# Performance work log

Measured on AMD Instinct MI355X. Metric: run time of the kernel, lower is better.

The kernel has to match this reference:

```python
import jax, jax.numpy as jnp
import numpy as np

B, C = 8, 2048          # batch, out_dim (projection channels)
HG = WG = 32            # global crop feature map
HL = WL = 12            # local crop feature map
STUDENT_TEMP = 0.1
TEMP_SCHEDULE = np.concatenate([np.linspace(0.04, 0.07, 30), np.ones(100 - 30) * 0.07])

# Fixed relative boxes (x1, x2, y1, y2) per (iq, v) crop pair, shared across the
# batch so grid shapes are static. Source computes grid_H from teacher_feat.shape[0]
# (= C, a quirk of the original code) and grid_W from shape[1] (= spatial H); boxes
# are chosen so resulting grids are ~[22-25, 22-24].
PAIRS = [
    (0, 1, (-0.80, 0.70, -0.500, -0.475), (-0.90, 0.60, -0.60, 0.60)),
    (0, 2, (-0.75, 0.75,  0.100,  0.125), (-0.80, 0.80, -0.80, 0.80)),
    (0, 3, (-0.60, 0.90, -0.200, -0.178), (-0.70, 0.90, -0.90, 0.70)),
    (1, 0, (-0.70, 0.80,  0.300,  0.322), (-0.85, 0.65, -0.50, 0.90)),
    (1, 2, (-0.90, 0.50, -0.100, -0.076), (-0.60, 0.95, -0.95, 0.60)),
    (1, 3, (-0.50, 0.95,  0.200,  0.224), (-0.90, 0.90, -0.40, 0.95)),
]


def _grid_dims(box, Hc, Wc):
    x1, x2, y1, y2 = box
    return int(abs(y1 - y2) / 2 * Hc), int(abs(x1 - x2) / 2 * Wc)  # (grid_H, grid_W)


def _make_grid(box, gH, gW):
    # Faithful to source: meshgrid([linspace(y1,y2,gH), linspace(x1,x2,gW)]),
    # stacked so channel 0 holds the y-linspace (which grid_sample reads as x).
    x1, x2, y1, y2 = box
    yy, xx = jnp.meshgrid(jnp.linspace(y1, y2, gH), jnp.linspace(x1, x2, gW), indexing='ij')
    return jnp.stack([yy, xx], axis=-1)  # [gH, gW, 2]


def _grid_sample_border(img, grid):
    # torch.nn.functional.grid_sample, bilinear, padding_mode='border',
    # align_corners=False. img: [B, C, H, W], grid: [gH, gW, 2] (same grid per batch).
    H, W = img.shape[-2], img.shape[-1]
    gx, gy = grid[..., 0], grid[..., 1]
    ix = jnp.clip((gx + 1.0) * (W * 0.5) - 0.5, 0.0, W - 1.0)  # border: clip coords
    iy = jnp.clip((gy + 1.0) * (H * 0.5) - 0.5, 0.0, H - 1.0)
    x0f, y0f = jnp.floor(ix), jnp.floor(iy)
    wx = (ix - x0f)[None, None]  # [1,1,gH,gW]
    wy = (iy - y0f)[None, None]
    x0 = x0f.astype(jnp.int32)
    y0 = y0f.astype(jnp.int32)
    x1 = jnp.minimum(x0 + 1, W - 1)
    y1 = jnp.minimum(y0 + 1, H - 1)
    v00 = img[:, :, y0, x0]
    v01 = img[:, :, y0, x1]
    v10 = img[:, :, y1, x0]
    v11 = img[:, :, y1, x1]
    return (1.0 - wy) * ((1.0 - wx) * v00 + wx * v01) + wy * ((1.0 - wx) * v10 + wx * v11)


def setup_inputs() -> dict:
    key = jax.random.key(0)
    ks = jax.random.split(key, 7)
    return {
        'student_g0': jax.random.normal(ks[0], (B, C, HG, WG), jnp.float32),
        'student_g1': jax.random.normal(ks[1], (B, C, HG, WG), jnp.float32),
        'student_l0': jax.random.normal(ks[2], (B, C, HL, WL), jnp.float32),
        'student_l1': jax.random.normal(ks[3], (B, C, HL, WL), jnp.float32),
        'teacher_g0': jax.random.normal(ks[4], (B, C, HG, WG), jnp.float32),
        'teacher_g1': jax.random.normal(ks[5], (B, C, HG, WG), jnp.float32),
        'center': jax.random.normal(ks[6], (1, C), jnp.float32) * 0.1,
        'epoch': 5,
    }


def reference(student_g0, student_g1, student_l0, student_l1,
              teacher_g0, teacher_g1, center, epoch):
    temp = float(TEMP_SCHEDULE[epoch])
    students = [s / STUDENT_TEMP for s in (student_g0, student_g1, student_l0, student_l1)]
    cen = center[:, :, None, None]  # [1,C,1,1]
    cteach = [jax.nn.softmax((t - cen) / temp, axis=1) for t in (teacher_g0, teacher_g1)]

    losses = []
    for iq, v, tbox, sbox in PAIRS:
        tfeat = cteach[iq]   # [B,C,H,W]
        sfeat = students[v]  # [B,C,h,w]
        # Faithful: source passes (shape[0]=C, shape[1]=spatial H) as (H, W).
        gH, gW = _grid_dims(tbox, C, tfeat.shape[2])
        t_common = jax.lax.stop_gradient(_grid_sample_border(tfeat, _make_grid(tbox, gH, gW)))
        s_common = _grid_sample_border(sfeat, _make_grid(sbox, gH, gW))
        # cross-entropy over channels -> [B, gH, gW]
        loss = (-t_common * jax.nn.log_softmax(s_common, axis=1)).sum(axis=1)
        losses.append(loss.reshape(-1))
    return jnp.concatenate(losses).mean()
```

## Files before the change

kernel.cpp:

```cpp
#include <hip/hip_runtime.h>
#include <hip/hip_fp16.h>

#define NPOS 26688

struct PairInfo {
  int iq, v, Hs, gH, gW, base, per;
  unsigned magicPer, magicW;
  int tOfs, tN, tCb;
  int sN, sCb;
  float tx1, tx2, ty1, ty2;
  float sx1, sx2, sy1, sy2;
};

__constant__ PairInfo g_pairs[6] = {
  {0,1,32,25,24,    0,600, 7158279u,178956971u,    0,2, 7, 22,5, -0.80f,0.70f,-0.500f,-0.475f,  -0.90f,0.60f,-0.60f,0.60f},
  {0,2,12,25,24, 4800,600, 7158279u,178956971u,  512,2,17, 12,0, -0.75f,0.75f, 0.100f, 0.125f,  -0.80f,0.80f,-0.80f,0.80f},
  {0,3,12,22,24, 9600,528, 8134408u,178956971u, 1024,2,12, 12,0, -0.60f,0.90f,-0.200f,-0.178f,  -0.70f,0.90f,-0.90f,0.70f},
  {1,0,32,22,24,13824,528, 8134408u,178956971u, 1536,2,20, 24,7, -0.70f,0.80f, 0.300f, 0.322f,  -0.85f,0.65f,-0.50f,0.90f},
  {1,2,12,24,22,18048,528, 8134408u,195225787u, 2048,3,13, 12,0, -0.90f,0.50f,-0.100f,-0.076f,  -0.60f,0.95f,-0.95f,0.60f},
  {1,3,12,24,23,22272,552, 7780739u,186737709u, 2816,3,18, 12,0, -0.50f,0.95f, 0.200f, 0.224f,  -0.90f,0.90f,-0.40f,0.95f},
};

__constant__ int g_ux[2][32] = {
  {-1,-1,-1,-1,-1,-1,-1, 0, 1,-1,-1,-1, 2, 3,-1,-1,-1, 4, 5,-1,-1,-1,-1,-1,-1,-1,-1,-1,-1,-1,-1,-1},
  {-1,-1,-1,-1,-1,-1,-1,-1,-1,-1,-1,-1,-1, 0, 1, 2,-1,-1, 3, 4, 5, 6,-1,-1,-1,-1,-1,-1,-1,-1,-1,-1},
};
__constant__ int g_tentX[2][8] = {
  { 7, 8,12,13,17,18,-100,-100},
  {13,14,15,18,19,20,  20,  21},
};
__constant__ int g_tentO[2][8] = {
  {   0,   0,1024,1024, 512, 512,   0,   0},
  {2048,2048,2048,2816,2816,2816,1536,1536},
};
__constant__ int g_tentN[2][8] = {
  {2,2,2,2,2,2,2,2},
  {3,3,3,3,3,3,2,2},
};
__constant__ int g_tentC[2][8] = {
  {0,1,0,1,0,1,0,0},
  {0,1,2,0,1,2,0,1},
};
__constant__ int g_cumTex[6] = {0, 512, 1024, 1536, 2048, 2816};
__constant__ int g_tN[6]    = {2, 2, 2, 2, 3, 3};
__constant__ int g_tCb[6]   = {7, 17, 12, 20, 13, 18};

__device__ inline float get_invtemp(const int* __restrict__ ep) {
  int e = ep[0];
  e = e < 0 ? 0 : (e > 99 ? 99 : e);
  float temp = (e < 30) ? (0.04f + (float)e * (0.03f / 29.0f)) : 0.07f;
  return 1.0f / temp;
}

__device__ inline float sel4(const float4& v, int q) {
  return q == 0 ? v.x : q == 1 ? v.y : q == 2 ? v.z : v.w;
}

typedef _Float16 hv2 __attribute__((ext_vector_type(2)));
__device__ inline float fdot2f(__half2 a, __half2 b, float c) {
#if defined(__has_builtin)
#if __has_builtin(__builtin_amdgcn_fdot2)
  return __builtin_amdgcn_fdot2(*reinterpret_cast<hv2*>(&a),
                                *reinterpret_cast<hv2*>(&b), c, false);
#else
  float2 af = __half22float2(a), bf = __half22float2(b);
  return fmaf(af.x, bf.x, fmaf(af.y, bf.y, c));
#endif
#else
  float2 af = __half22float2(a), bf = __half22float2(b);
  return fmaf(af.x, bf.x, fmaf(af.y, bf.y, c));
#endif
}

__global__ __launch_bounds__(256) void dino_phase1(
    const float* __restrict__ tg0, const float* __restrict__ tg1,
    const float* __restrict__ cen, const int* __restrict__ ep,
    float* __restrict__ part_m, float* __restrict__ part_s,
    __half* __restrict__ Tc,
    const float* __restrict__ sl0, const float* __restrict__ sl1,
    __half* __restrict__ Sl0, __half* __restrict__ Sl1,
    const float* __restrict__ sg0, const float* __restrict__ sg1,
    __half* __restrict__ Sg0, __half* __restrict__ Sg1) {
  __shared__ float smem[7424];
  int bid = blockIdx.x;
  int t = threadIdx.x;

  if (bid < 1024) {
    int cg = bid & 63;
    int b = (bid >> 6) & 7;
    int view = bid >> 9;
    const float* __restrict__ src = view ? tg1 : tg0;
    float invtemp = get_invtemp(ep);
    float* cenl = smem + 7392;
    if (t < 32) cenl[t] = cen[cg * 32 + t];
    __syncthreads();

    int y = t >> 3, x0 = (t & 7) * 4;
    int y33 = y * 33;
    int s0 = g_ux[view][x0], s1 = g_ux[view][x0 + 1];
    int s2 = g_ux[view][x0 + 2], s3 = g_ux[view][x0 + 3];
    const float* base = src + ((size_t)(b * 2048 + cg * 32)) * 1024 + t * 4;

    float4 m4 = make_float4(-1e30f, -1e30f, -1e30f, -1e30f);
    float4 s4 = make_float4(0.f, 0.f, 0.f, 0.f);
#pragma unroll 4
    for (int c = 0; c < 32; ++c) {
      float4 v = *reinterpret_cast<const float4*>(base + (size_t)c * 1024);
      float cv = cenl[c];
      float4 lg;
      lg.x = (v.x - cv) * invtemp; lg.y = (v.y - cv) * invtemp;
      lg.z = (v.z - cv) * invtemp; lg.w = (v.w - cv) * invtemp;
      if (s0 >= 0) smem[s0 * 1056 + y33 + c] = lg.x;
      if (s1 >= 0) smem[s1 * 1056 + y33 + c] = lg.y;
      if (s2 >= 0) smem[s2 * 1056 + y33 + c] = lg.z;
      if (s3 >= 0) smem[s3 * 1056 + y33 + c] = lg.w;
      float mn;
      mn = fmaxf(m4.x, lg.x); s4.x = s4.x * __expf(m4.x - mn) + __expf(lg.x - mn); m4.x = mn;
      mn = fmaxf(m4.y, lg.y); s4.y = s4.y * __expf(m4.y - mn) + __expf(lg.y - mn); m4.y = mn;
      mn = fmaxf(m4.z, lg.z); s4.z = s4.z * __expf(m4.z - mn) + __expf(lg.z - mn); m4.z = mn;
      mn = fmaxf(m4.w, lg.w); s4.w = s4.w * __expf(m4.w - mn) + __expf(lg.w - mn); m4.w = mn;
    }
    size_t prow = ((size_t)((view * 8 + b) * 64 + cg)) * 1024 + t * 4;
    *reinterpret_cast<float4*>(part_m + prow) = m4;
    *reinterpret_cast<float4*>(part_s + prow) = s4;

#pragma unroll
    for (int e = 0; e < 8; ++e) {
      int ex = g_tentX[view][e];
      int d = ex - x0;
      if (d >= 0 && d < 4) {
        int slot = g_ux[view][ex];
        float mm = sel4(m4, d);
        int tex = g_tentO[view][e] + (b * 32 + y) * g_tentN[view][e] + g_tentC[view][e];
        tex = min(max(tex, 0), 3583);
        __half hv[32];
#pragma unroll
        for (int c = 0; c < 32; ++c)
          hv[c] = __float2half(smem[slot * 1056 + y33 + c] - mm);
        uint4* dst = reinterpret_cast<uint4*>(Tc + (size_t)tex * 2048 + cg * 32);
        const uint4* sv = reinterpret_cast<const uint4*>(hv);
        dst[0] = sv[0]; dst[1] = sv[1]; dst[2] = sv[2]; dst[3] = sv[3];
      }
    }
    return;
  }

  if (bid < 3072) {
    float* tile = smem;
    int lb = bid - 1024;
    int ct = lb & 127;
    int g = lb >> 7;
    int b = g & 7;
    int vv = g >> 3;
    const float* __restrict__ src = vv ? sl1 : sl0;
    __half* __restrict__ dst = vv ? Sl1 : Sl0;
    const float* sp = src + ((size_t)(b * 2048 + ct * 16)) * 144;
#pragma unroll
    for (int k = 0; k < 9; ++k) {
      int idx = t + 256 * k;
      int c = idx / 144;
      int yx = idx - c * 144;
      tile[c * 145 + yx] = sp[idx] * 10.f;
    }
    __syncthreads();
    __half* dp = dst + ((size_t)(b * 144)) * 2048 + ct * 16;
#pragma unroll
    for (int k = 0; k < 2; ++k) {
      int u = t + 256 * k;
      if (u < 288) {
        int yx = u >> 1, q8 = (u & 1) * 8;
        __half hv[8];
#pragma unroll
        for (int j = 0; j < 8; ++j) hv[j] = __float2half(tile[(q8 + j) * 145 + yx]);
        *reinterpret_cast<float4*>(dp + (size_t)yx * 2048 + q8) =
            *reinterpret_cast<float4*>(hv);
      }
    }
    return;
  }

  float* tile = smem;
  int lb = bid - 3072;
  int ct = lb & 31;
  int t2 = lb >> 5;
  int yi = t2 % 26;
  int g = t2 / 26;
  int y = yi + 1;
  int b = g & 7;
  int which = g >> 3;
  const float* __restrict__ src = which ? sg1 : sg0;
  __half* __restrict__ dst = which ? Sg1 : Sg0;
  int cb = which ? 5 : 7;
  int n = which ? 22 : 24;

  int xg = t & 7, ch = t >> 3;
  const float* sp = src + (((size_t)(b * 2048 + ct * 64 + ch)) * 32 + y) * 32 + xg * 4;
  float4 v0 = *reinterpret_cast<const float4*>(sp);
  float4 v1 = *reinterpret_cast<const float4*>(sp + 32768);
  tile[ch * 33 + xg * 4 + 0] = v0.x * 10.f;
  tile[ch * 33 + xg * 4 + 1] = v0.y * 10.f;
  tile[ch * 33 + xg * 4 + 2] = v0.z * 10.f;
  tile[ch * 33 + xg * 4 + 3] = v0.w * 10.f;
  tile[(ch + 32) * 33 + xg * 4 + 0] = v1.x * 10.f;
  tile[(ch + 32) * 33 + xg * 4 + 1] = v1.y * 10.f;
  tile[(ch + 32) * 33 + xg * 4 + 2] = v1.z * 10.f;
  tile[(ch + 32) * 33 + xg * 4 + 3] = v1.w * 10.f;
  __syncthreads();
  int xx = t >> 3, ccq = (t & 7) * 8;
  if (xx >= cb && xx < cb + n) {
    __half hv[8];
#pragma unroll
    for (int j = 0; j < 8; ++j) hv[j] = __float2half(tile[(ccq + j) * 33 + xx]);
    __half* dp = dst + ((size_t)((b * 32 + y) * n + (xx - cb))) * 2048 + ct * 64 + ccq;
    *reinterpret_cast<float4*>(dp) = *reinterpret_cast<float4*>(hv);
  }
}

union H8 { uint4 u; __half2 h[4]; };

__global__ __launch_bounds__(256) void dino_probs(
    const __half* __restrict__ Tc, __half* __restrict__ Tp,
    const float* __restrict__ part_m, const float* __restrict__ part_s) {
  __shared__ float pr[66];
  int bid = blockIdx.x;
  int t = threadIdx.x;
  int p = 0;
#pragma unroll
  for (int q = 1; q < 6; ++q) p += (bid >= g_cumTex[q]) ? 1 : 0;
  int r = bid - g_cumTex[p];
  int n = g_tN[p];
  int by = (n == 2) ? (r >> 1) : (r / 3);
  by = min(max(by, 0), 255);
  int ci = min(max(r - by * n, 0), n - 1);
  int x = g_tCb[p] + ci;
  int view = (p >= 3) ? 1 : 0;
  int b = by >> 5, y = by & 31;
  int vb = view * 8 + b;

  if (t < 64) {
    float mg = part_m[((size_t)(vb * 64 + t)) * 1024 + y * 32 + x];
    float sg = part_s[((size_t)(vb * 64 + t)) * 1024 + y * 32 + x];
    pr[t] = mg;
    float M = mg;
#pragma unroll
    for (int off = 32; off; off >>= 1) M = fmaxf(M, __shfl_xor(M, off));
    float sv = sg * __expf(mg - M);
#pragma unroll
    for (int off = 32; off; off >>= 1) sv += __shfl_xor(sv, off);
    if (t == 0) { pr[64] = M; pr[65] = 1.f / sv; }
  }
  __syncthreads();
  float off = pr[t >> 2] - pr[64];
  float invS = pr[65];

  int tex = min(g_cumTex[p] + by * n + ci, 3583);
  size_t base = (size_t)tex * 2048 + t * 8;
  H8 hh;
  hh.u = *reinterpret_cast<const uint4*>(Tc + base);
#pragma unroll
  for (int pc = 0; pc < 4; ++pc) {
    float2 f = __half22float2(hh.h[pc]);
    f.x = __expf(f.x + off) * invS;
    f.y = __expf(f.y + off) * invS;
    hh.h[pc] = __floats2half2_rn(f.x, f.y);
  }
  *reinterpret_cast<uint4*>(Tp + base) = hh.u;
}

__global__ __launch_bounds__(256) void dino_main(
    const __half* __restrict__ Tp,
    const __half* __restrict__ S0, const __half* __restrict__ S1,
    const __half* __restrict__ S2, const __half* __restrict__ S3,
    float* __restrict__ losses) {
  int wid = threadIdx.x >> 6, lane = threadIdx.x & 63;
  int pair = blockIdx.x / 1200;
  int slot = blockIdx.x - pair * 1200;
  PairInfo pi = g_pairs[pair];
  int posInPair = slot * 4 + wid;
  if (posInPair >= pi.per * 8) return;

  unsigned up = (unsigned)posInPair;
  int b = (int)__umulhi(up, pi.magicPer);
  b = min(max(b, 0), 7);
  int r = posInPair - b * pi.per;
  r = min(max(r, 0), pi.per - 1);
  int i = (int)__umulhi((unsigned)r, pi.magicW);
  i = min(max(i, 0), pi.gH - 1);
  int j = r - i * pi.gW;
  j = min(max(j, 0), pi.gW - 1);

  float tyy = pi.ty1 + (float)i * (pi.ty2 - pi.ty1) / (float)(pi.gH - 1);
  float txx = pi.tx1 + (float)j * (pi.tx2 - pi.tx1) / (float)(pi.gW - 1);
  float tix = fminf(fmaxf((tyy + 1.0f) * 16.0f - 0.5f, 0.0f), 31.0f);
  float tiy = fminf(fmaxf((txx + 1.0f) * 16.0f - 0.5f, 0.0f), 31.0f);
  int tx0 = (int)tix, ty0 = (int)tiy;
  float wxt = tix - (float)tx0, wyt = tiy - (float)ty0;
  int tx1i = min(tx0 + 1, 31), ty1i = min(ty0 + 1, 31);

  int hs = pi.Hs;
  float hh = 0.5f * (float)hs, hm = (float)(hs - 1);
  float syy = pi.sy1 + (float)i * (pi.sy2 - pi.sy1) / (float)(pi.gH - 1);
  float sxx = pi.sx1 + (float)j * (pi.sx2 - pi.sx1) / (float)(pi.gW - 1);
  float six = fminf(fmaxf((syy + 1.0f) * hh - 0.5f, 0.0f), hm);
  float siy = fminf(fmaxf((sxx + 1.0f) * hh - 0.5f, 0.0f), hm);
  int sx0 = (int)six, sy0 = (int)siy;
  float wxs = six - (float)sx0, wys = siy - (float)sy0;
  int sx1i = min(sx0 + 1, hs - 1), sy1i = min(sy0 + 1, hs - 1);

  const __half* __restrict__ S =
      (pi.v == 0) ? S0 : (pi.v == 1) ? S1 : (pi.v == 2) ? S2 : S3;

  int tc0 = min(max(tx0 - pi.tCb, 0), pi.tN - 1);
  int tc1 = min(max(tx1i - pi.tCb, 0), pi.tN - 1);
  int trow = pi.tOfs + (b * 32 + ty0) * pi.tN;
  int trow1 = pi.tOfs + (b * 32 + ty1i) * pi.tN;
  int toff00 = min(trow + tc0, 3583) * 2048;
  int toff01 = min(trow + tc1, 3583) * 2048;
  int toff10 = min(trow1 + tc0, 3583) * 2048;
  int toff11 = min(trow1 + tc1, 3583) * 2048;
  int sc0 = min(max(sx0 - pi.sCb, 0), pi.sN - 1);
  int sc1 = min(max(sx1i - pi.sCb, 0), pi.sN - 1);
  int soff00 = ((b * hs + sy0) * pi.sN + sc0) * 2048;
  int soff01 = ((b * hs + sy0) * pi.sN + sc1) * 2048;
  int soff10 = ((b * hs + sy1i) * pi.sN + sc0) * 2048;
  int soff11 = ((b * hs + sy1i) * pi.sN + sc1) * 2048;

  __half2 wt00 = __float2half2_rn((1.f - wyt) * (1.f - wxt));
  __half2 wt01 = __float2half2_rn((1.f - wyt) * wxt);
  __half2 wt10 = __float2half2_rn(wyt * (1.f - wxt));
  __half2 wt11 = __float2half2_rn(wyt * wxt);
  __half2 ws00 = __float2half2_rn((1.f - wys) * (1.f - wxs));
  __half2 ws01 = __float2half2_rn((1.f - wys) * wxs);
  __half2 ws10 = __float2half2_rn(wys * (1.f - wxs));
  __half2 ws11 = __float2half2_rn(wys * wxs);

  float sum = 0.f, dot = 0.f;
#pragma unroll
  for (int k = 0; k < 4; ++k) {
    int c0 = (k << 9) + (lane << 3);
    H8 t00, t01, t10, t11, a00, a01, a10, a11;
    t00.u = *reinterpret_cast<const uint4*>(Tp + toff00 + c0);
    t01.u = *reinterpret_cast<const uint4*>(Tp + toff01 + c0);
    t10.u = *reinterpret_cast<const uint4*>(Tp + toff10 + c0);
    t11.u = *reinterpret_cast<const uint4*>(Tp + toff11 + c0);
    a00.u = *reinterpret_cast<const uint4*>(S + soff00 + c0);
    a01.u = *reinterpret_cast<const uint4*>(S + soff01 + c0);
    a10.u = *reinterpret_cast<const uint4*>(S + soff10 + c0);
    a11.u = *reinterpret_cast<const uint4*>(S + soff11 + c0);
#pragma unroll
    for (int p = 0; p < 4; ++p) {
      __half2 tc2 = __hmul2(wt00, t00.h[p]);
      tc2 = __hfma2(wt01, t01.h[p], tc2);
      tc2 = __hfma2(wt10, t10.h[p], tc2);
      tc2 = __hfma2(wt11, t11.h[p], tc2);
      __half2 sc2 = __hmul2(ws00, a00.h[p]);
      sc2 = __hfma2(ws01, a01.h[p], sc2);
      sc2 = __hfma2(ws10, a10.h[p], sc2);
      sc2 = __hfma2(ws11, a11.h[p], sc2);
      dot = fdot2f(tc2, sc2, dot);
      float2 scf = __half22float2(sc2);
      sum += __expf(scf.x);
      sum += __expf(scf.y);
    }
  }
#pragma unroll
  for (int off = 32; off; off >>= 1) {
    sum += __shfl_down(sum, off);
    dot += __shfl_down(dot, off);
  }
  if (lane == 0) losses[pi.base + posInPair] = logf(sum) - dot;
}

__global__ __launch_bounds__(1024) void dino_reduce(const float* __restrict__ losses,
                                                    float* __restrict__ out) {
  __shared__ double sd[1024];
  int t = threadIdx.x;
  double a = 0.0;
  for (int i4 = t; i4 < 6672; i4 += 1024) {
    float4 v = *reinterpret_cast<const float4*>(losses + i4 * 4);
    a += (double)v.x + (double)v.y + (double)v.z + (double)v.w;
  }
  sd[t] = a;
  __syncthreads();
  for (int off = 512; off; off >>= 1) {
    if (t < off) sd[t] += sd[t + off];
    __syncthreads();
  }
  if (t == 0) out[0] = (float)(sd[0] / (double)NPOS);
}

extern "C" void kernel_launch(void* const* d_in, const int* in_sizes, int n_in,
                              void* d_out, int out_size, void* d_ws, size_t ws_size,
                              hipStream_t stream) {
  const float* sg0 = (const float*)d_in[0];
  const float* sg1 = (const float*)d_in[1];
  const float* sl0 = (const float*)d_in[2];
  const float* sl1 = (const float*)d_in[3];
  const float* tg0 = (const float*)d_in[4];
  const float* tg1 = (const float*)d_in[5];
  const float* cen = (const float*)d_in[6];
  const int* epoch = (const int*)d_in[7];
  float* out = (float*)d_out;
  char* w = (char*)d_ws;

  const size_t OFF_LOSS= 131072;
  const size_t OFF_PM  = 262144;
  const size_t OFF_PS  = 4456448;
  const size_t OFF_TC  = 8650752;
  const size_t OFF_TP  = 23330816;
  const size_t OFF_SG0 = 38010880;
  const size_t OFF_SG1 = 63176704;
  const size_t OFF_SL0 = 86245376;
  const size_t OFF_SL1 = 90963968;

  float* losses = (float*)(w + OFF_LOSS);
  float* part_m = (float*)(w + OFF_PM);
  float* part_s = (float*)(w + OFF_PS);
  __half* Tc  = (__half*)(w + OFF_TC);
  __half* Tp  = (__half*)(w + OFF_TP);
  __half* Sg0 = (__half*)(w + OFF_SG0);
  __half* Sg1 = (__half*)(w + OFF_SG1);
  __half* Sl0 = (__half*)(w + OFF_SL0);
  __half* Sl1 = (__half*)(w + OFF_SL1);

  dino_phase1<<<16384, 256, 0, stream>>>(tg0, tg1, cen, epoch, part_m, part_s, Tc,
                                         sl0, sl1, Sl0, Sl1, sg0, sg1, Sg0, Sg1);
  dino_probs<<<3584, 256, 0, stream>>>(Tc, Tp, part_m, part_s);
  dino_main<<<7200, 256, 0, stream>>>(Tp, Sg0, Sg1, Sl0, Sl1, losses);
  dino_reduce<<<1, 1024, 0, stream>>>(losses, out);
}
```

Measured before the change: 122.6 us.

## Compute teacher softmax only at sampled columns instead of full per-pixel partial stats

Phase 1 no longer computes online max/sum partials over every teacher pixel. It only gathers the raw fp32 teacher values at the few x-columns the grid samples. The probs kernel now does the full channel softmax (with centering and temperature) per sampled position, in one block-wide reduction. The global-student transpose is also restructured to process 16 channels by the full 32x32 map per block, so far fewer phase-1 blocks are launched. This removes the exp-heavy work and the part_m/part_s traffic for unused pixels, at the cost of a larger fp32 intermediate buffer.

After: 142.2 us. +16.0%, slower.

```diff
diff --git a/kernel.cpp b/kernel.cpp
--- a/kernel.cpp
+++ b/kernel.cpp
@@ -25,35 +25,17 @@
   {-1,-1,-1,-1,-1,-1,-1, 0, 1,-1,-1,-1, 2, 3,-1,-1,-1, 4, 5,-1,-1,-1,-1,-1,-1,-1,-1,-1,-1,-1,-1,-1},
   {-1,-1,-1,-1,-1,-1,-1,-1,-1,-1,-1,-1,-1, 0, 1, 2,-1,-1, 3, 4, 5, 6,-1,-1,-1,-1,-1,-1,-1,-1,-1,-1},
 };
-__constant__ int g_tentX[2][8] = {
-  { 7, 8,12,13,17,18,-100,-100},
-  {13,14,15,18,19,20,  20,  21},
-};
-__constant__ int g_tentO[2][8] = {
-  {   0,   0,1024,1024, 512, 512,   0,   0},
-  {2048,2048,2048,2816,2816,2816,1536,1536},
-};
-__constant__ int g_tentN[2][8] = {
-  {2,2,2,2,2,2,2,2},
-  {3,3,3,3,3,3,2,2},
-};
-__constant__ int g_tentC[2][8] = {
-  {0,1,0,1,0,1,0,0},
-  {0,1,2,0,1,2,0,1},
-};
-__constant__ int g_cumTex[6] = {0, 512, 1024, 1536, 2048, 2816};
-__constant__ int g_tN[6]    = {2, 2, 2, 2, 3, 3};
-__constant__ int g_tCb[6]   = {7, 17, 12, 20, 13, 18};
+__constant__ int g_weSlot[2][8] = {{0,1,2,3,4,5,0,0},{0,1,2,3,4,5,5,6}};
+__constant__ int g_weBase[2][8] = {{0,1,1024,1025,512,513,0,0},
+                                   {2048,2049,2050,2816,2817,2818,1536,1537}};
+__constant__ int g_weStr[2][8]  = {{2,2,2,2,2,2,2,2},{3,3,3,3,3,3,2,2}};
+__constant__ int g_weN[2] = {6, 8};
 
 __device__ inline float get_invtemp(const int* __restrict__ ep) {
   int e = ep[0];
   e = e < 0 ? 0 : (e > 99 ? 99 : e);
   float temp = (e < 30) ? (0.04f + (float)e * (0.03f / 29.0f)) : 0.07f;
   return 1.0f / temp;
-}
-
-__device__ inline float sel4(const float4& v, int q) {
-  return q == 0 ? v.x : q == 1 ? v.y : q == 2 ? v.z : v.w;
 }
 
 typedef _Float16 hv2 __attribute__((ext_vector_type(2)));
@@ -74,198 +56,184 @@
 
 __global__ __launch_bounds__(256) void dino_phase1(
     const float* __restrict__ tg0, const float* __restrict__ tg1,
-    const float* __restrict__ cen, const int* __restrict__ ep,
-    float* __restrict__ part_m, float* __restrict__ part_s,
-    __half* __restrict__ Tc,
+    float* __restrict__ Tcf,
+    const float* __restrict__ sg0, const float* __restrict__ sg1,
+    __half* __restrict__ Sg0, __half* __restrict__ Sg1,
     const float* __restrict__ sl0, const float* __restrict__ sl1,
-    __half* __restrict__ Sl0, __half* __restrict__ Sl1,
-    const float* __restrict__ sg0, const float* __restrict__ sg1,
-    __half* __restrict__ Sg0, __half* __restrict__ Sg1) {
-  __shared__ float smem[7424];
+    __half* __restrict__ Sl0, __half* __restrict__ Sl1) {
+  __shared__ float smem[5700];
   int bid = blockIdx.x;
   int t = threadIdx.x;
 
-  if (bid < 1024) {
-    int cg = bid & 63;
-    int b = (bid >> 6) & 7;
-    int view = bid >> 9;
+  if (bid < 2048) {
+    int cg = bid & 127;
+    int b = (bid >> 7) & 7;
+    int view = bid >> 10;
     const float* __restrict__ src = view ? tg1 : tg0;
-    float invtemp = get_invtemp(ep);
-    float* cenl = smem + 7392;
-    if (t < 32) cenl[t] = cen[cg * 32 + t];
+    const float* base = src + ((size_t)(b * 2048 + cg * 16)) * 1024;
+#pragma unroll
+    for (int k = 0; k < 16; ++k) {
+      int idx = k * 256 + t;
+      int c = idx >> 8, p4 = idx & 255;
+      int y = p4 >> 3, x0 = (p4 & 7) * 4;
+      float4 v = *reinterpret_cast<const float4*>(base + (size_t)c * 1024 + p4 * 4);
+      int s0 = g_ux[view][x0],     s1 = g_ux[view][x0 + 1];
+      int s2 = g_ux[view][x0 + 2], s3 = g_ux[view][x0 + 3];
+      if (s0 >= 0) smem[s0 * 544 + y * 17 + c] = v.x;
+      if (s1 >= 0) smem[s1 * 544 + y * 17 + c] = v.y;
+      if (s2 >= 0) smem[s2 * 544 + y * 17 + c] = v.z;
+      if (s3 >= 0) smem[s3 * 544 + y * 17 + c] = v.w;
+    }
     __syncthreads();
-
-    int y = t >> 3, x0 = (t & 7) * 4;
-    int y33 = y * 33;
-    int s0 = g_ux[view][x0], s1 = g_ux[view][x0 + 1];
-    int s2 = g_ux[view][x0 + 2], s3 = g_ux[view][x0 + 3];
-    const float* base = src + ((size_t)(b * 2048 + cg * 32)) * 1024 + t * 4;
-
-    float4 m4 = make_float4(-1e30f, -1e30f, -1e30f, -1e30f);
-    float4 s4 = make_float4(0.f, 0.f, 0.f, 0.f);
-#pragma unroll 4
-    for (int c = 0; c < 32; ++c) {
-      float4 v = *reinterpret_cast<const float4*>(base + (size_t)c * 1024);
-      float cv = cenl[c];
-      float4 lg;
-      lg.x = (v.x - cv) * invtemp; lg.y = (v.y - cv) * invtemp;
-      lg.z = (v.z - cv) * invtemp; lg.w = (v.w - cv) * invtemp;
-      if (s0 >= 0) smem[s0 * 1056 + y33 + c] = lg.x;
-      if (s1 >= 0) smem[s1 * 1056 + y33 + c] = lg.y;
-      if (s2 >= 0) smem[s2 * 1056 + y33 + c] = lg.z;
-      if (s3 >= 0) smem[s3 * 1056 + y33 + c] = lg.w;
-      float mn;
-      mn = fmaxf(m4.x, lg.x); s4.x = s4.x * __expf(m4.x - mn) + __expf(lg.x - mn); m4.x = mn;
-      mn = fmaxf(m4.y, lg.y); s4.y = s4.y * __expf(m4.y - mn) + __expf(lg.y - mn); m4.y = mn;
-      mn = fmaxf(m4.z, lg.z); s4.z = s4.z * __expf(m4.z - mn) + __expf(lg.z - mn); m4.z = mn;
-      mn = fmaxf(m4.w, lg.w); s4.w = s4.w * __expf(m4.w - mn) + __expf(lg.w - mn); m4.w = mn;
-    }
-    size_t prow = ((size_t)((view * 8 + b) * 64 + cg)) * 1024 + t * 4;
-    *reinterpret_cast<float4*>(part_m + prow) = m4;
-    *reinterpret_cast<float4*>(part_s + prow) = s4;
-
-#pragma unroll
-    for (int e = 0; e < 8; ++e) {
-      int ex = g_tentX[view][e];
-      int d = ex - x0;
-      if (d >= 0 && d < 4) {
-        int slot = g_ux[view][ex];
-        float mm = sel4(m4, d);
-        int tex = g_tentO[view][e] + (b * 32 + y) * g_tentN[view][e] + g_tentC[view][e];
-        tex = min(max(tex, 0), 3583);
-        __half hv[32];
-#pragma unroll
-        for (int c = 0; c < 32; ++c)
-          hv[c] = __float2half(smem[slot * 1056 + y33 + c] - mm);
-        uint4* dst = reinterpret_cast<uint4*>(Tc + (size_t)tex * 2048 + cg * 32);
-        const uint4* sv = reinterpret_cast<const uint4*>(hv);
-        dst[0] = sv[0]; dst[1] = sv[1]; dst[2] = sv[2]; dst[3] = sv[3];
+    int nw = g_weN[view];
+    if (t < nw * 32) {
+      int e = t >> 5, y = t & 31;
+      int slot = g_weSlot[view][e];
+      int tex = g_weBase[view][e] + (b * 32 + y) * g_weStr[view][e];
+      tex = min(max(tex, 0), 3583);
+      float arr[16];
+#pragma unroll
+      for (int c = 0; c < 16; ++c) arr[c] = smem[slot * 544 + y * 17 + c];
+      float* dp = Tcf + (size_t)tex * 2048 + cg * 16;
+#pragma unroll
+      for (int q = 0; q < 4; ++q)
+        *reinterpret_cast<float4*>(dp + q * 4) =
+            make_float4(arr[4 * q], arr[4 * q + 1], arr[4 * q + 2], arr[4 * q + 3]);
+    }
+    return;
+  }
+
+  if (bid < 4096) {
+    int lb = bid - 2048;
+    int cg = lb & 127;
+    int b = (lb >> 7) & 7;
+    int which = lb >> 10;
+    const float* __restrict__ src = which ? sg1 : sg0;
+    __half* __restrict__ dst = which ? Sg1 : Sg0;
+    int cb = which ? 5 : 7;
+    int n = which ? 22 : 24;
+    unsigned magicN = which ? 195225787u : 178956971u;
+    const float* base = src + ((size_t)(b * 2048 + cg * 16)) * 1024;
+    __half* hlds = reinterpret_cast<__half*>(smem);
+#pragma unroll
+    for (int k = 0; k < 16; ++k) {
+      int idx = k * 256 + t;
+      int c = idx >> 8, p4 = idx & 255;
+      int y = p4 >> 3, x0 = (p4 & 7) * 4;
+      float4 v = *reinterpret_cast<const float4*>(base + (size_t)c * 1024 + p4 * 4);
+      if (y >= 1 && y <= 26) {
+        int rb = (y - 1) * n - cb;
+#pragma unroll
+        for (int q = 0; q < 4; ++q) {
+          int x = x0 + q;
+          if (x >= cb && x < cb + n) {
+            float val = (q == 0) ? v.x : (q == 1) ? v.y : (q == 2) ? v.z : v.w;
+            hlds[(rb + x) * 18 + c] = __float2half(val * 10.f);
+          }
+        }
       }
     }
+    __syncthreads();
+    int total = 26 * n;
+    const unsigned* hw = reinterpret_cast<const unsigned*>(smem);
+#pragma unroll
+    for (int k2 = 0; k2 < 3; ++k2) {
+      int u = t + 256 * k2;
+      if (u < total) {
+        int yy = (int)__umulhi((unsigned)u, magicN);
+        int cx = u - yy * n;
+        int y = yy + 1;
+        unsigned r[8];
+#pragma unroll
+        for (int q = 0; q < 8; ++q) r[q] = hw[u * 9 + q];
+        unsigned* dp = reinterpret_cast<unsigned*>(
+            dst + ((size_t)((b * 32 + y) * n + cx)) * 2048 + cg * 16);
+        *reinterpret_cast<uint4*>(dp) = make_uint4(r[0], r[1], r[2], r[3]);
+        *reinterpret_cast<uint4*>(dp + 4) = make_uint4(r[4], r[5], r[6], r[7]);
+      }
+    }
     return;
   }
 
-  if (bid < 3072) {
-    float* tile = smem;
-    int lb = bid - 1024;
-    int ct = lb & 127;
-    int g = lb >> 7;
-    int b = g & 7;
-    int vv = g >> 3;
-    const float* __restrict__ src = vv ? sl1 : sl0;
-    __half* __restrict__ dst = vv ? Sl1 : Sl0;
-    const float* sp = src + ((size_t)(b * 2048 + ct * 16)) * 144;
-#pragma unroll
-    for (int k = 0; k < 9; ++k) {
-      int idx = t + 256 * k;
-      int c = idx / 144;
-      int yx = idx - c * 144;
-      tile[c * 145 + yx] = sp[idx] * 10.f;
-    }
-    __syncthreads();
-    __half* dp = dst + ((size_t)(b * 144)) * 2048 + ct * 16;
-#pragma unroll
-    for (int k = 0; k < 2; ++k) {
-      int u = t + 256 * k;
-      if (u < 288) {
-        int yx = u >> 1, q8 = (u & 1) * 8;
-        __half hv[8];
-#pragma unroll
-        for (int j = 0; j < 8; ++j) hv[j] = __float2half(tile[(q8 + j) * 145 + yx]);
-        *reinterpret_cast<float4*>(dp + (size_t)yx * 2048 + q8) =
-            *reinterpret_cast<float4*>(hv);
-      }
-    }
-    return;
-  }
-
   float* tile = smem;
-  int lb = bid - 3072;
-  int ct = lb & 31;
-  int t2 = lb >> 5;
-  int yi = t2 % 26;
-  int g = t2 / 26;
-  int y = yi + 1;
+  int lb = bid - 4096;
+  int ct = lb & 127;
+  int g = lb >> 7;
   int b = g & 7;
-  int which = g >> 3;
-  const float* __restrict__ src = which ? sg1 : sg0;
-  __half* __restrict__ dst = which ? Sg1 : Sg0;
-  int cb = which ? 5 : 7;
-  int n = which ? 22 : 24;
-
-  int xg = t & 7, ch = t >> 3;
-  const float* sp = src + (((size_t)(b * 2048 + ct * 64 + ch)) * 32 + y) * 32 + xg * 4;
-  float4 v0 = *reinterpret_cast<const float4*>(sp);
-  float4 v1 = *reinterpret_cast<const float4*>(sp + 32768);
-  tile[ch * 33 + xg * 4 + 0] = v0.x * 10.f;
-  tile[ch * 33 + xg * 4 + 1] = v0.y * 10.f;
-  tile[ch * 33 + xg * 4 + 2] = v0.z * 10.f;
-  tile[ch * 33 + xg * 4 + 3] = v0.w * 10.f;
-  tile[(ch + 32) * 33 + xg * 4 + 0] = v1.x * 10.f;
-  tile[(ch + 32) * 33 + xg * 4 + 1] = v1.y * 10.f;
-  tile[(ch + 32) * 33 + xg * 4 + 2] = v1.z * 10.f;
-  tile[(ch + 32) * 33 + xg * 4 + 3] = v1.w * 10.f;
+  int vv = g >> 3;
+  const float* __restrict__ src = vv ? sl1 : sl0;
+  __half* __restrict__ dst = vv ? Sl1 : Sl0;
+  const float* sp = src + ((size_t)(b * 2048 + ct * 16)) * 144;
+#pragma unroll
+  for (int k = 0; k < 9; ++k) {
+    int idx = t + 256 * k;
+    int c = idx / 144;
+    int yx = idx - c * 144;
+    tile[c * 145 + yx] = sp[idx] * 10.f;
+  }
   __syncthreads();
-  int xx = t >> 3, ccq = (t & 7) * 8;
-  if (xx >= cb && xx < cb + n) {
-    __half hv[8];
-#pragma unroll
-    for (int j = 0; j < 8; ++j) hv[j] = __float2half(tile[(ccq + j) * 33 + xx]);
-    __half* dp = dst + ((size_t)((b * 32 + y) * n + (xx - cb))) * 2048 + ct * 64 + ccq;
-    *reinterpret_cast<float4*>(dp) = *reinterpret_cast<float4*>(hv);
-  }
+  __half* dp = dst + ((size_t)(b * 144)) * 2048 + ct * 16;
+#pragma unroll
+  for (int k = 0; k < 2; ++k) {
+    int u = t + 256 * k;
+    if (u < 288) {
+      int yx = u >> 1, q8 = (u & 1) * 8;
+      __half hv[8];
+#pragma unroll
+      for (int j = 0; j < 8; ++j) hv[j] = __float2half(tile[(q8 + j) * 145 + yx]);
+      *reinterpret_cast<float4*>(dp + (size_t)yx * 2048 + q8) =
+          *reinterpret_cast<float4*>(hv);
+    }
+  }
+}
+
+__global__ __launch_bounds__(256) void dino_probs(
+    const float* __restrict__ Tcf, __half* __restrict__ Tp,
+    const float* __restrict__ cen, const int* __restrict__ ep) {
+  __shared__ float rm[4], rs[4];
+  int tex = blockIdx.x;
+  int t = threadIdx.x;
+  int lane = t & 63, w = t >> 6;
+  float invtemp = get_invtemp(ep);
+
+  const float* cp = Tcf + (size_t)tex * 2048 + t * 8;
+  float4 v0 = *reinterpret_cast<const float4*>(cp);
+  float4 v1 = *reinterpret_cast<const float4*>(cp + 4);
+  float4 c0 = *reinterpret_cast<const float4*>(cen + t * 8);
+  float4 c1 = *reinterpret_cast<const float4*>(cen + t * 8 + 4);
+  float lg[8];
+  lg[0] = (v0.x - c0.x) * invtemp; lg[1] = (v0.y - c0.y) * invtemp;
+  lg[2] = (v0.z - c0.z) * invtemp; lg[3] = (v0.w - c0.w) * invtemp;
+  lg[4] = (v1.x - c1.x) * invtemp; lg[5] = (v1.y - c1.y) * invtemp;
+  lg[6] = (v1.z - c1.z) * invtemp; lg[7] = (v1.w - c1.w) * invtemp;
+
+  float m = lg[0];
+#pragma unroll
+  for (int q = 1; q < 8; ++q) m = fmaxf(m, lg[q]);
+#pragma unroll
+  for (int off = 32; off; off >>= 1) m = fmaxf(m, __shfl_xor(m, off));
+  if (lane == 0) rm[w] = m;
+  __syncthreads();
+  float M = fmaxf(fmaxf(rm[0], rm[1]), fmaxf(rm[2], rm[3]));
+
+  float e[8];
+  float s = 0.f;
+#pragma unroll
+  for (int q = 0; q < 8; ++q) { e[q] = __expf(lg[q] - M); s += e[q]; }
+#pragma unroll
+  for (int off = 32; off; off >>= 1) s += __shfl_xor(s, off);
+  if (lane == 0) rs[w] = s;
+  __syncthreads();
+  float invS = 1.f / (rs[0] + rs[1] + rs[2] + rs[3]);
+
+  __half o[8];
+#pragma unroll
+  for (int q = 0; q < 8; ++q) o[q] = __float2half(e[q] * invS);
+  *reinterpret_cast<uint4*>(Tp + (size_t)tex * 2048 + t * 8) =
+      *reinterpret_cast<uint4*>(o);
 }
 
 union H8 { uint4 u; __half2 h[4]; };
-
-__global__ __launch_bounds__(256) void dino_probs(
-    const __half* __restrict__ Tc, __half* __restrict__ Tp,
-    const float* __restrict__ part_m, const float* __restrict__ part_s) {
-  __shared__ float pr[66];
-  int bid = blockIdx.x;
-  int t = threadIdx.x;
-  int p = 0;
-#pragma unroll
-  for (int q = 1; q < 6; ++q) p += (bid >= g_cumTex[q]) ? 1 : 0;
-  int r = bid - g_cumTex[p];
-  int n = g_tN[p];
-  int by = (n == 2) ? (r >> 1) : (r / 3);
-  by = min(max(by, 0), 255);
-  int ci = min(max(r - by * n, 0), n - 1);
-  int x = g_tCb[p] + ci;
-  int view = (p >= 3) ? 1 : 0;
-  int b = by >> 5, y = by & 31;
-  int vb = view * 8 + b;
-
-  if (t < 64) {
-    float mg = part_m[((size_t)(vb * 64 + t)) * 1024 + y * 32 + x];
-    float sg = part_s[((size_t)(vb * 64 + t)) * 1024 + y * 32 + x];
-    pr[t] = mg;
-    float M = mg;
-#pragma unroll
-    for (int off = 32; off; off >>= 1) M = fmaxf(M, __shfl_xor(M, off));
-    float sv = sg * __expf(mg - M);
-#pragma unroll
-    for (int off = 32; off; off >>= 1) sv += __shfl_xor(sv, off);
-    if (t == 0) { pr[64] = M; pr[65] = 1.f / sv; }
-  }
-  __syncthreads();
-  float off = pr[t >> 2] - pr[64];
-  float invS = pr[65];
-
-  int tex = min(g_cumTex[p] + by * n + ci, 3583);
-  size_t base = (size_t)tex * 2048 + t * 8;
-  H8 hh;
-  hh.u = *reinterpret_cast<const uint4*>(Tc + base);
-#pragma unroll
-  for (int pc = 0; pc < 4; ++pc) {
-    float2 f = __half22float2(hh.h[pc]);
-    f.x = __expf(f.x + off) * invS;
-    f.y = __expf(f.y + off) * invS;
-    hh.h[pc] = __floats2half2_rn(f.x, f.y);
-  }
-  *reinterpret_cast<uint4*>(Tp + base) = hh.u;
-}
 
 __global__ __launch_bounds__(256) void dino_main(
     const __half* __restrict__ Tp,
@@ -403,29 +371,25 @@
   float* out = (float*)d_out;
   char* w = (char*)d_ws;
 
-  const size_t OFF_LOSS= 131072;
-  const size_t OFF_PM  = 262144;
-  const size_t OFF_PS  = 4456448;
-  const size_t OFF_TC  = 8650752;
-  const size_t OFF_TP  = 23330816;
-  const size_t OFF_SG0 = 38010880;
-  const size_t OFF_SG1 = 63176704;
-  const size_t OFF_SL0 = 86245376;
-  const size_t OFF_SL1 = 90963968;
+  const size_t OFF_LOSS = 131072;
+  const size_t OFF_TCF  = 262144;
+  const size_t OFF_TP   = 29622272;
+  const size_t OFF_SG0  = 44302336;
+  const size_t OFF_SG1  = 69468160;
+  const size_t OFF_SL0  = 92536832;
+  const size_t OFF_SL1  = 97255424;
 
   float* losses = (float*)(w + OFF_LOSS);
-  float* part_m = (float*)(w + OFF_PM);
-  float* part_s = (float*)(w + OFF_PS);
-  __half* Tc  = (__half*)(w + OFF_TC);
+  float* Tcf = (float*)(w + OFF_TCF);
   __half* Tp  = (__half*)(w + OFF_TP);
   __half* Sg0 = (__half*)(w + OFF_SG0);
   __half* Sg1 = (__half*)(w + OFF_SG1);
   __half* Sl0 = (__half*)(w + OFF_SL0);
   __half* Sl1 = (__half*)(w + OFF_SL1);
 
-  dino_phase1<<<16384, 256, 0, stream>>>(tg0, tg1, cen, epoch, part_m, part_s, Tc,
-                                         sl0, sl1, Sl0, Sl1, sg0, sg1, Sg0, Sg1);
-  dino_probs<<<3584, 256, 0, stream>>>(Tc, Tp, part_m, part_s);
+  dino_phase1<<<6144, 256, 0, stream>>>(tg0, tg1, Tcf, sg0, sg1, Sg0, Sg1,
+                                        sl0, sl1, Sl0, Sl1);
+  dino_probs<<<3584, 256, 0, stream>>>(Tcf, Tp, cen, epoch);
   dino_main<<<7200, 256, 0, stream>>>(Tp, Sg0, Sg1, Sl0, Sl1, losses);
   dino_reduce<<<1, 1024, 0, stream>>>(losses, out);
 }
```
